# Performance work log

Hardware: AMD Instinct MI355X
Metric: run time of the kernel (lower is better)

Reference implementation:

```python
import jax, jax.numpy as jnp
import numpy as np

N_P, N_A, N_S, D = 50000, 25000, 1, 64
ALPHA = 0.2  # leaky_relu negative slope
E_P2P, E_P2A, E_A2P, E_A2A = 800000, 400000, 400000, 400000


def _gat(z_msg, wh_dst, aw, src, dst, n_dst):
    """Per-edge-type GAT: score = leaky_relu(attn_fc([z_src ; Wh_dst])),
    segment softmax over destination, weighted scatter-sum of z_src.
    Attention linear is split into src/dst halves and applied per-node (cheaper)."""
    d = z_msg.shape[1]
    e = (z_msg @ aw[:d])[src] + (wh_dst @ aw[d:])[dst]  # [E]
    e = jnp.where(e > 0, e, ALPHA * e)                   # leaky_relu
    m = jax.ops.segment_max(e, dst, num_segments=n_dst)
    ex = jnp.exp(e - m[dst])
    den = jax.ops.segment_sum(ex, dst, num_segments=n_dst)
    w = ex / den[dst]                                    # per-dst softmax (mailbox softmax)
    return jax.ops.segment_sum(w[:, None] * z_msg[src], dst, num_segments=n_dst)


def setup_inputs() -> dict:
    ks = jax.random.split(jax.random.key(0), 32)
    sc = 1.0 / np.sqrt(D)
    f32, i32 = jnp.float32, jnp.int32
    inp = {
        "feat_P": jax.random.normal(ks[0], (N_P, D), f32),
        "feat_A": jax.random.normal(ks[1], (N_A, D), f32),
        "feat_state": jax.random.normal(ks[2], (N_S, D), f32),
    }
    for i, n in enumerate(["P", "A", "p2p", "p2a", "a2p", "a2a", "p2s", "a2s", "in"]):
        inp["W_" + n] = jax.random.normal(ks[3 + i], (D, D), f32) * sc
        inp["b_" + n] = jnp.zeros((D,), f32)
    for i, n in enumerate(["p2p", "p2a", "a2p", "a2a", "p2s", "a2s"]):
        inp["a_" + n] = jax.random.normal(ks[12 + i], (2 * D,), f32) * sc
    inp["src_p2p"] = jax.random.randint(ks[18], (E_P2P,), 0, N_P, i32)
    inp["dst_p2p"] = jax.random.randint(ks[19], (E_P2P,), 0, N_P, i32)
    inp["src_p2a"] = jax.random.randint(ks[20], (E_P2A,), 0, N_P, i32)
    inp["dst_p2a"] = jax.random.randint(ks[21], (E_P2A,), 0, N_A, i32)
    inp["src_a2p"] = jax.random.randint(ks[22], (E_A2P,), 0, N_A, i32)
    inp["dst_a2p"] = jax.random.randint(ks[23], (E_A2P,), 0, N_P, i32)
    inp["src_a2a"] = jax.random.randint(ks[24], (E_A2A,), 0, N_A, i32)
    inp["dst_a2a"] = jax.random.randint(ks[25], (E_A2A,), 0, N_A, i32)
    inp["src_p2s"] = jnp.arange(N_P, dtype=i32)
    inp["dst_p2s"] = jnp.zeros((N_P,), i32)
    inp["src_a2s"] = jnp.arange(N_A, dtype=i32)
    inp["dst_a2s"] = jnp.zeros((N_A,), i32)
    return inp


def reference(feat_P, feat_A, feat_state,
              W_P, b_P, W_A, b_A, W_p2p, b_p2p, W_p2a, b_p2a, W_a2p, b_a2p,
              W_a2a, b_a2a, W_p2s, b_p2s, W_a2s, b_a2s, W_in, b_in,
              a_p2p, a_p2a, a_a2p, a_a2a, a_p2s, a_a2s,
              src_p2p, dst_p2p, src_p2a, dst_p2a, src_a2p, dst_a2p,
              src_a2a, dst_a2a, src_p2s, dst_p2s, src_a2s, dst_a2s):
    Wh_P = feat_P @ W_P + b_P          # self transform per node type
    Wh_A = feat_A @ W_A + b_A
    Wh_in = feat_state @ W_in + b_in   # 'in' self-loop message to state
    h_P = jax.nn.relu(
        Wh_P
        + _gat(feat_P @ W_p2p + b_p2p, Wh_P, a_p2p, src_p2p, dst_p2p, N_P)
        + _gat(feat_A @ W_a2p + b_a2p, Wh_P, a_a2p, src_a2p, dst_a2p, N_P))
    h_A = jax.nn.relu(
        Wh_A
        + _gat(feat_P @ W_p2a + b_p2a, Wh_A, a_p2a, src_p2a, dst_p2a, N_A)
        + _gat(feat_A @ W_a2a + b_a2a, Wh_A, a_a2a, src_a2a, dst_a2a, N_A))
    h_S = jax.nn.relu(
        Wh_in
        + _gat(feat_P @ W_p2s + b_p2s, Wh_in, a_p2s, src_p2s, dst_p2s, N_S)
        + _gat(feat_A @ W_a2s + b_a2s, Wh_in, a_a2s, src_a2s, dst_a2s, N_S))
    return (h_P, h_A, h_S)
```

## Files before the change

### kernel.cpp

```cpp
#include <hip/hip_runtime.h>
#include <math.h>

#define ALPHA 0.2f
#define NP 50000
#define NA 25000
#define NBINS 150000
#define ABASE 100000
#define NBUCK 586
#define CH 4096
#define CAP 8192
#define GP ((NP + 63) / 64)
#define GA ((NA + 63) / 64)
#define GATB ((NP + NA) / 4)
#define SNB_P 128
#define SNB_A 64
#define SNB (SNB_P + SNB_A)

typedef unsigned short u16;
typedef __attribute__((ext_vector_type(8))) short bf16x8;
typedef __attribute__((ext_vector_type(8))) unsigned short u16x8;
typedef __attribute__((ext_vector_type(4))) float f32x4;

__device__ __forceinline__ float bf2f(u16 u) { return __uint_as_float(((unsigned)u) << 16); }
__device__ __forceinline__ u16 f2bf(float f) {
    unsigned x = __float_as_uint(f);
    return (u16)((x + 0x7fffu + ((x >> 16) & 1u)) >> 16);
}

struct FrontArgs {
    const float *feat_P, *feat_A, *feat_S;
    const float *W_P, *b_P, *W_A, *b_A, *W_p2p, *b_p2p, *W_p2a, *b_p2a,
                *W_a2p, *b_a2p, *W_a2a, *b_a2a, *W_p2s, *b_p2s, *W_a2s, *b_a2s,
                *W_in, *b_in;
    const float *a_p2p, *a_p2a, *a_a2p, *a_a2a, *a_p2s, *a_a2s;
    float *WhP, *WhA;
    u16 *z_p2p, *z_p2a, *z_p2s, *z_a2p, *z_a2a, *z_a2s;
    float *ss_p2p, *sd_p2p, *ss_p2a, *sd_p2a, *ss_a2p, *sd_a2p, *ss_a2a, *sd_a2a,
          *ss_p2s, *ss_a2s;
    float *sdst2, *outS, *den2, *numP, *numA;
    int *done;
};

__device__ __forceinline__ void xform_body(int bid,
    const float* __restrict__ X, int N,
    const float* __restrict__ W0, const float* __restrict__ b0, float* __restrict__ Wh,
    const float* __restrict__ dA, float* __restrict__ sdA,
    const float* __restrict__ dB, float* __restrict__ sdB,
    const float* __restrict__ W1, const float* __restrict__ b1, u16* __restrict__ z1,
    const float* __restrict__ v1, float* __restrict__ s1,
    const float* __restrict__ W2, const float* __restrict__ b2, u16* __restrict__ z2,
    const float* __restrict__ v2, float* __restrict__ s2,
    const float* __restrict__ W3, const float* __restrict__ b3, u16* __restrict__ z3,
    const float* __restrict__ v3, float* __restrict__ s3)
{
    int tid = threadIdx.x, wv = tid >> 6, lane = tid & 63;
    int g = lane >> 4, li = lane & 15;
    const float* Wm = wv == 0 ? W0 : wv == 1 ? W1 : wv == 2 ? W2 : W3;
    const float* bm = wv == 0 ? b0 : wv == 1 ? b1 : wv == 2 ? b2 : b3;
    const float* dv = wv == 0 ? dA : wv == 1 ? v1 : wv == 2 ? v2 : v3;
    float* sm       = wv == 0 ? sdA : wv == 1 ? s1 : wv == 2 ? s2 : s3;
    u16* zm         = wv == 1 ? z1 : wv == 2 ? z2 : wv == 3 ? z3 : nullptr;

    bf16x8 Bf[4][2];
#pragma unroll
    for (int cb = 0; cb < 4; ++cb)
#pragma unroll
        for (int kc = 0; kc < 2; ++kc) {
            bf16x8 t;
#pragma unroll
            for (int j = 0; j < 8; ++j)
                t[j] = (short)f2bf(Wm[(kc * 32 + g * 8 + j) * 64 + cb * 16 + li]);
            Bf[cb][kc] = t;
        }
    float bl[4], dvl[4], dbl[4];
#pragma unroll
    for (int cb = 0; cb < 4; ++cb) {
        bl[cb]  = bm[cb * 16 + li];
        dvl[cb] = dv[cb * 16 + li];
        dbl[cb] = (wv == 0) ? dB[cb * 16 + li] : 0.f;
    }

    int base0 = bid * 64;
#pragma unroll
    for (int rt = 0; rt < 4; ++rt) {
        int rbase = base0 + rt * 16;
        if (rbase >= N) break;
        int rowC = min(rbase + li, N - 1);
        bf16x8 Af[2];
#pragma unroll
        for (int kc = 0; kc < 2; ++kc) {
            const float* xp = X + (long long)rowC * 64 + kc * 32 + g * 8;
            float4 x0 = *(const float4*)xp;
            float4 x1 = *(const float4*)(xp + 4);
            bf16x8 t;
            t[0] = (short)f2bf(x0.x); t[1] = (short)f2bf(x0.y);
            t[2] = (short)f2bf(x0.z); t[3] = (short)f2bf(x0.w);
            t[4] = (short)f2bf(x1.x); t[5] = (short)f2bf(x1.y);
            t[6] = (short)f2bf(x1.z); t[7] = (short)f2bf(x1.w);
            Af[kc] = t;
        }
        f32x4 acc[4] = {{0,0,0,0},{0,0,0,0},{0,0,0,0},{0,0,0,0}};
#pragma unroll
        for (int kc = 0; kc < 2; ++kc)
#pragma unroll
            for (int cb = 0; cb < 4; ++cb)
                acc[cb] = __builtin_amdgcn_mfma_f32_16x16x32_bf16(Af[kc], Bf[cb][kc], acc[cb], 0, 0, 0);
        float pd[4] = {0,0,0,0}, pb[4] = {0,0,0,0};
#pragma unroll
        for (int cb = 0; cb < 4; ++cb)
#pragma unroll
            for (int r = 0; r < 4; ++r) {
                float val = acc[cb][r] + bl[cb];
                acc[cb][r] = val;
                pd[r] = fmaf(val, dvl[cb], pd[r]);
                pb[r] = fmaf(val, dbl[cb], pb[r]);
            }
#pragma unroll
        for (int o = 1; o < 16; o <<= 1)
#pragma unroll
            for (int r = 0; r < 4; ++r) {
                pd[r] += __shfl_xor(pd[r], o, 64);
                pb[r] += __shfl_xor(pb[r], o, 64);
            }
        int rg = rbase + g * 4;
        if (li == 0) {
#pragma unroll
            for (int r = 0; r < 4; ++r) {
                int row = rg + r;
                if (row < N) {
                    sm[row] = pd[r];
                    if (wv == 0) sdB[row] = pb[r];
                }
            }
        }
        if (wv == 0) {
#pragma unroll
            for (int r = 0; r < 4; ++r) {
                int row = rg + r;
                if (row < N)
#pragma unroll
                    for (int cb = 0; cb < 4; ++cb)
                        Wh[(long long)row * 64 + cb * 16 + li] = acc[cb][r];
            }
        } else {
#pragma unroll
            for (int r = 0; r < 4; ++r) {
                int row = rg + r;
                if (row < N)
#pragma unroll
                    for (int cb = 0; cb < 4; ++cb)
                        zm[(long long)row * 64 + cb * 16 + li] = f2bf(acc[cb][r]);
            }
        }
    }
}

__device__ __forceinline__ void edge_decode(int k,
    const int* __restrict__ s0, const int* __restrict__ d0, int E0,
    const int* __restrict__ s1, const int* __restrict__ d1, int E1,
    const int* __restrict__ s2, const int* __restrict__ d2, int E2,
    const int* __restrict__ s3, const int* __restrict__ d3,
    int& src, int& bin) {
    if (k < E0) { src = s0[k]; bin = 2 * d0[k]; return; }
    k -= E0; if (k < E1) { src = s1[k]; bin = 2 * d1[k] + 1; return; }
    k -= E1; if (k < E2) { src = s2[k]; bin = ABASE + 2 * d2[k]; return; }
    k -= E2; src = s3[k]; bin = ABASE + 2 * d3[k] + 1;
}

__global__ __launch_bounds__(256) void fused_front(FrontArgs A) {
    int bid = blockIdx.x;
    int tid = threadIdx.x;
    if (bid < GP) {
        xform_body(bid, A.feat_P, NP,
                   A.W_P, A.b_P, A.WhP, A.a_p2p + 64, A.sd_p2p, A.a_a2p + 64, A.sd_a2p,
                   A.W_p2p, A.b_p2p, A.z_p2p, A.a_p2p, A.ss_p2p,
                   A.W_p2a, A.b_p2a, A.z_p2a, A.a_p2a, A.ss_p2a,
                   A.W_p2s, A.b_p2s, A.z_p2s, A.a_p2s, A.ss_p2s);
        return;
    }
    bid -= GP;
    if (bid < GA) {
        xform_body(bid, A.feat_A, NA,
                   A.W_A, A.b_A, A.WhA, A.a_p2a + 64, A.sd_p2a, A.a_a2a + 64, A.sd_a2a,
                   A.W_a2p, A.b_a2p, A.z_a2p, A.a_a2p, A.ss_a2p,
                   A.W_a2a, A.b_a2a, A.z_a2a, A.a_a2a, A.ss_a2a,
                   A.W_a2s, A.b_a2s, A.z_a2s, A.a_a2s, A.ss_a2s);
        return;
    }
    if (tid < 64) {
        int c = tid;
        float acc = A.b_in[c];
        for (int k = 0; k < 64; ++k) acc = fmaf(A.feat_S[k], A.W_in[k * 64 + c], acc);
        A.outS[c] = acc;
        float v0 = acc * A.a_p2s[64 + c];
        float v1 = acc * A.a_a2s[64 + c];
#pragma unroll
        for (int off = 32; off > 0; off >>= 1) {
            v0 += __shfl_down(v0, off, 64);
            v1 += __shfl_down(v1, off, 64);
        }
        if (c == 0) { A.sdst2[0] = v0; A.sdst2[1] = v1; }
    } else if (tid < 128) A.numP[tid - 64] = 0.f;
    else if (tid < 192)   A.numA[tid - 128] = 0.f;
    else if (tid == 192)  A.den2[0] = 0.f;
    else if (tid == 193)  A.den2[1] = 0.f;
    else if (tid == 194)  *A.done = 0;
}

__global__ __launch_bounds__(256) void passA_scatter(
    const int* __restrict__ s0, const int* __restrict__ d0, int E0,
    const int* __restrict__ s1, const int* __restrict__ d1, int E1,
    const int* __restrict__ s2, const int* __restrict__ d2, int E2,
    const int* __restrict__ s3, const int* __restrict__ d3, int E3,
    int* __restrict__ cursor0, int Etot, int* __restrict__ ebuf) {
    __shared__ int h[NBUCK];
    __shared__ int base[NBUCK];
    int tid = threadIdx.x;
    for (int i = tid; i < NBUCK; i += 256) h[i] = 0;
    __syncthreads();
    int b0 = blockIdx.x * CH;
    int b1 = min(b0 + CH, Etot);
    int cbin[16], csrc[16];
#pragma unroll
    for (int it = 0; it < 16; ++it) {
        int i = b0 + it * 256 + tid;
        int bin = -1, src = 0;
        if (i < b1)
            edge_decode(i, s0, d0, E0, s1, d1, E1, s2, d2, E2, s3, d3, src, bin);
        cbin[it] = bin; csrc[it] = src;
        if (bin >= 0) atomicAdd(&h[bin >> 8], 1);
    }
    __syncthreads();
    for (int i = tid; i < NBUCK; i += 256) {
        int c = h[i];
        base[i] = c ? (i * CAP + atomicAdd(&cursor0[i], c)) : 0;
        h[i] = 0;
    }
    __syncthreads();
#pragma unroll
    for (int it = 0; it < 16; ++it) {
        int bin = cbin[it];
        if (bin >= 0) {
            int bk = bin >> 8;
            int pos = base[bk] + atomicAdd(&h[bk], 1);
            if (pos < (bk + 1) * CAP)
                ebuf[pos] = csrc[it] | ((bin & 255) << 16);
        }
    }
}

__global__ __launch_bounds__(256) void fine_sort(
    const int* __restrict__ ebuf, const int* __restrict__ cursor0,
    int* __restrict__ ssrc, int* __restrict__ offs) {
    __shared__ int lsrc[CAP];
    __shared__ int lcnt[256];
    __shared__ int loff[256];
    __shared__ int lcur[256];
    __shared__ int wtot[4];
    int b = blockIdx.x;
    int tid = threadIdx.x, lane = tid & 63, wv = tid >> 6;
    int bstart = b * CAP;
    int cnt = min(cursor0[b], CAP);
    int bend = bstart + cnt;
    lcnt[tid] = 0;
    __syncthreads();
    for (int e = bstart + tid; e < bend; e += 256)
        atomicAdd(&lcnt[((unsigned)ebuf[e]) >> 16], 1);
    __syncthreads();
    int v = lcnt[tid];
    int x = v;
#pragma unroll
    for (int o = 1; o < 64; o <<= 1) {
        int y = __shfl_up(x, o, 64);
        if (lane >= o) x += y;
    }
    if (lane == 63) wtot[wv] = x;
    __syncthreads();
    int woff = 0;
    for (int j = 0; j < wv; ++j) woff += wtot[j];
    int excl = x + woff - v;
    loff[tid] = excl;
    lcur[tid] = excl;
    __syncthreads();
    for (int e = bstart + tid; e < bend; e += 256) {
        int val = ebuf[e];
        int pos = atomicAdd(&lcur[((unsigned)val) >> 16], 1);
        lsrc[pos] = val & 0xFFFF;
    }
    __syncthreads();
    for (int i = tid; i < cnt; i += 256) ssrc[bstart + i] = lsrc[i];
    offs[b * 257 + tid] = bstart + loff[tid];
    if (tid == 0) offs[b * 257 + 256] = bend;
}

__device__ __forceinline__ void seg_gat_g8(const int* __restrict__ ssrc, int s0, int s1,
                                           const float* __restrict__ ss, float sd,
                                           const u16* __restrict__ z, int lane,
                                           float* __restrict__ acc) {
    int cnt = s1 - s0;
    if (cnt <= 0) return;
    int egrp = lane >> 3, cg8 = (lane & 7) * 8;
    float den = 0.f;
    for (int i = s0 + lane; i < s1; i += 64) {
        float e = ss[ssrc[i]] + sd; e = e > 0.f ? e : ALPHA * e; den += __expf(e);
    }
#pragma unroll
    for (int o = 32; o > 0; o >>= 1) den += __shfl_xor(den, o, 64);
    float inv = 1.f / den;
    for (int c = s0; c < s1; c += 64) {
        int i = c + lane; int s = 0; float w = 0.f;
        if (i < s1) {
            s = ssrc[i];
            float e = ss[s] + sd; e = e > 0.f ? e : ALPHA * e;
            w = __expf(e) * inv;
        }
        int cc = min(64, s1 - c);
        int nit = (cc + 7) >> 3;
        for (int it = 0; it < nit; ++it) {
            int ei = it * 8 + egrp;
            float wt = __shfl(w, ei, 64);
            int   st = __shfl(s, ei, 64);
            u16x8 q = *(const u16x8*)(z + (long long)st * 64 + cg8);
#pragma unroll
            for (int j = 0; j < 8; ++j)
                acc[j] = fmaf(wt, bf2f(q[j]), acc[j]);
        }
    }
}

__global__ __launch_bounds__(256) void fused_back(
    const int* __restrict__ ssrc, const int* __restrict__ offs,
    const float* __restrict__ WhP, float* __restrict__ outP,
    const float* __restrict__ WhA, float* __restrict__ outA,
    const float* __restrict__ ss_p2p, const float* __restrict__ sd_p2p, const u16* __restrict__ z_p2p,
    const float* __restrict__ ss_a2p, const float* __restrict__ sd_a2p, const u16* __restrict__ z_a2p,
    const float* __restrict__ ss_p2a, const float* __restrict__ sd_p2a, const u16* __restrict__ z_p2a,
    const float* __restrict__ ss_a2a, const float* __restrict__ sd_a2a, const u16* __restrict__ z_a2a,
    const int* __restrict__ srcP, const float* __restrict__ ssP, const u16* __restrict__ zP, int EP,
    const int* __restrict__ srcA, const float* __restrict__ ssA, const u16* __restrict__ zA, int EA,
    const float* __restrict__ sdst2, float* __restrict__ numP, float* __restrict__ numA,
    float* __restrict__ den2, int* __restrict__ done, float* __restrict__ outS) {
    int tid = threadIdx.x, lane = tid & 63, wv = tid >> 6;
    if ((int)blockIdx.x >= SNB) {
        int g = ((int)blockIdx.x - SNB) * 4 + wv;
        bool isP = g < NP;
        int d = isP ? g : g - NP;
        int bin0 = isP ? 2 * d : ABASE + 2 * d;
        int obase = (bin0 >> 8) * 257 + (bin0 & 255);
        int e0 = offs[obase], e1 = offs[obase + 1], e2 = offs[obase + 2];
        int cnt = e2 - e0, c1 = e1 - e0;
        const float* ss0 = isP ? ss_p2p : ss_p2a;
        const float* ss1 = isP ? ss_a2p : ss_a2a;
        const u16* z0 = isP ? z_p2p : z_p2a;
        const u16* z1 = isP ? z_a2p : z_a2a;
        float sd0v = (isP ? sd_p2p : sd_p2a)[d];
        float sd1v = (isP ? sd_a2p : sd_a2a)[d];
        int egrp = lane >> 3, cg8 = (lane & 7) * 8;
        float acc[8] = {0.f, 0.f, 0.f, 0.f, 0.f, 0.f, 0.f, 0.f};
        if (cnt <= 64) {
            int s = 0; float w = 0.f;
            bool s1f = lane >= c1;
            if (lane < cnt) {
                s = ssrc[e0 + lane];
                float sc = (s1f ? ss1[s] : ss0[s]) + (s1f ? sd1v : sd0v);
                sc = sc > 0.f ? sc : ALPHA * sc;
                w = __expf(sc);
            }
            float d0 = s1f ? 0.f : w, d1 = s1f ? w : 0.f;
#pragma unroll
            for (int o = 32; o > 0; o >>= 1) {
                d0 += __shfl_xor(d0, o, 64);
                d1 += __shfl_xor(d1, o, 64);
            }
            float inv0 = 1.f / d0, inv1 = 1.f / d1;
            w = (lane < cnt) ? w * (s1f ? inv1 : inv0) : 0.f;
            int nit = (cnt + 7) >> 3;
            float wtv[8]; int stv[8]; u16x8 q[8];
#pragma unroll
            for (int it = 0; it < 8; ++it)
                if (it < nit) {
                    int ei = it * 8 + egrp;
                    wtv[it] = __shfl(w, ei, 64);
                    stv[it] = __shfl(s, ei, 64);
                }
#pragma unroll
            for (int it = 0; it < 8; ++it)
                if (it < nit) {
                    const u16* zp = (it * 8 + egrp >= c1) ? z1 : z0;
                    q[it] = *(const u16x8*)(zp + (long long)stv[it] * 64 + cg8);
                }
#pragma unroll
            for (int it = 0; it < 8; ++it)
                if (it < nit) {
#pragma unroll
                    for (int j = 0; j < 8; ++j)
                        acc[j] = fmaf(wtv[it], bf2f(q[it][j]), acc[j]);
                }
        } else {
            seg_gat_g8(ssrc, e0, e1, ss0, sd0v, z0, lane, acc);
            seg_gat_g8(ssrc, e1, e2, ss1, sd1v, z1, lane, acc);
        }
#pragma unroll
        for (int o = 8; o <= 32; o <<= 1)
#pragma unroll
            for (int j = 0; j < 8; ++j)
                acc[j] += __shfl_xor(acc[j], o, 64);
        if (lane < 8) {
            const float* Wh = isP ? WhP : WhA;
            float* outp = isP ? outP : outA;
            const float* sp = &Wh[(long long)d * 64 + lane * 8];
            float4 s0v = *(const float4*)sp;
            float4 s1v = *(const float4*)(sp + 4);
            float4 r0, r1;
            r0.x = fmaxf(s0v.x + acc[0], 0.f); r0.y = fmaxf(s0v.y + acc[1], 0.f);
            r0.z = fmaxf(s0v.z + acc[2], 0.f); r0.w = fmaxf(s0v.w + acc[3], 0.f);
            r1.x = fmaxf(s1v.x + acc[4], 0.f); r1.y = fmaxf(s1v.y + acc[5], 0.f);
            r1.z = fmaxf(s1v.z + acc[6], 0.f); r1.w = fmaxf(s1v.w + acc[7], 0.f);
            float* op = &outp[(long long)d * 64 + lane * 8];
            *(float4*)op = r0;
            *(float4*)(op + 4) = r1;
        }
        return;
    }
    __shared__ float red[4][64];
    __shared__ float dred[4];
    __shared__ int tick;
    int sb = blockIdx.x;
    bool isP = sb < SNB_P;
    const int* src = isP ? srcP : srcA;
    const float* ss = isP ? ssP : ssA;
    const u16* z = isP ? zP : zA;
    int E = isP ? EP : EA;
    float sdst = sdst2[isP ? 0 : 1];
    float* num = isP ? numP : numA;
    int bidl = isP ? sb : sb - SNB_P;
    int nb = isP ? SNB_P : SNB_A;
    int egrp = lane >> 3, cg8 = (lane & 7) * 8;
    int gw = bidl * 4 + wv;
    int waves = nb * 4;
    float acc[8] = {0,0,0,0,0,0,0,0};
    float dpart = 0.f;
    for (int base = gw * 8; base < E; base += waves * 8) {
        int i = base + egrp;
        float w = 0.f; int ri = 0;
        if (i < E) {
            ri = src[i];
            float e = ss[ri] + sdst;
            e = e > 0.f ? e : ALPHA * e;
            w = __expf(e);
        }
        dpart += w;
        u16x8 q = *(const u16x8*)(z + (long long)ri * 64 + cg8);
#pragma unroll
        for (int j = 0; j < 8; ++j)
            acc[j] = fmaf(w, bf2f(q[j]), acc[j]);
    }
#pragma unroll
    for (int o = 8; o <= 32; o <<= 1)
#pragma unroll
        for (int j = 0; j < 8; ++j)
            acc[j] += __shfl_xor(acc[j], o, 64);
#pragma unroll
    for (int o = 32; o > 0; o >>= 1) dpart += __shfl_xor(dpart, o, 64);
    if (lane < 8)
#pragma unroll
        for (int j = 0; j < 8; ++j) red[wv][lane * 8 + j] = acc[j];
    if (lane == 0) dred[wv] = dpart;
    __syncthreads();
    if (tid < 64) {
        float t = red[0][tid] + red[1][tid] + red[2][tid] + red[3][tid];
        atomicAdd(&num[tid], t);
    }
    if (tid == 64) {
        float dtot = (dred[0] + dred[1] + dred[2] + dred[3]) * 0.125f;
        atomicAdd(&den2[isP ? 0 : 1], dtot);
    }
    __threadfence();
    __syncthreads();
    if (tid == 0) tick = atomicAdd(done, 1);
    __syncthreads();
    if (tick == SNB - 1 && tid < 64) {
        float dP = __hip_atomic_load(&den2[0], __ATOMIC_ACQUIRE, __HIP_MEMORY_SCOPE_AGENT);
        float dA = __hip_atomic_load(&den2[1], __ATOMIC_ACQUIRE, __HIP_MEMORY_SCOPE_AGENT);
        float nP = __hip_atomic_load(&numP[tid], __ATOMIC_ACQUIRE, __HIP_MEMORY_SCOPE_AGENT);
        float nA = __hip_atomic_load(&numA[tid], __ATOMIC_ACQUIRE, __HIP_MEMORY_SCOPE_AGENT);
        float whin = outS[tid];
        outS[tid] = fmaxf(whin + nP / dP + nA / dA, 0.f);
    }
}

extern "C" void kernel_launch(void* const* d_in, const int* in_sizes, int n_in,
                              void* d_out, int out_size, void* d_ws, size_t ws_size,
                              hipStream_t stream) {
    const float* feat_P = (const float*)d_in[0];
    const float* feat_A = (const float*)d_in[1];
    const float* feat_S = (const float*)d_in[2];
    const float* W_P   = (const float*)d_in[3];  const float* b_P   = (const float*)d_in[4];
    const float* W_A   = (const float*)d_in[5];  const float* b_A   = (const float*)d_in[6];
    const float* W_p2p = (const float*)d_in[7];  const float* b_p2p = (const float*)d_in[8];
    const float* W_p2a = (const float*)d_in[9];  const float* b_p2a = (const float*)d_in[10];
    const float* W_a2p = (const float*)d_in[11]; const float* b_a2p = (const float*)d_in[12];
    const float* W_a2a = (const float*)d_in[13]; const float* b_a2a = (const float*)d_in[14];
    const float* W_p2s = (const float*)d_in[15]; const float* b_p2s = (const float*)d_in[16];
    const float* W_a2s = (const float*)d_in[17]; const float* b_a2s = (const float*)d_in[18];
    const float* W_in  = (const float*)d_in[19]; const float* b_in  = (const float*)d_in[20];
    const float* a_p2p = (const float*)d_in[21];
    const float* a_p2a = (const float*)d_in[22];
    const float* a_a2p = (const float*)d_in[23];
    const float* a_a2a = (const float*)d_in[24];
    const float* a_p2s = (const float*)d_in[25];
    const float* a_a2s = (const float*)d_in[26];
    const int* src_p2p = (const int*)d_in[27]; const int* dst_p2p = (const int*)d_in[28];
    const int* src_p2a = (const int*)d_in[29]; const int* dst_p2a = (const int*)d_in[30];
    const int* src_a2p = (const int*)d_in[31]; const int* dst_a2p = (const int*)d_in[32];
    const int* src_a2a = (const int*)d_in[33]; const int* dst_a2a = (const int*)d_in[34];
    const int* src_p2s = (const int*)d_in[35];
    const int* src_a2s = (const int*)d_in[37];
    int E_p2p = in_sizes[27], E_p2a = in_sizes[29], E_a2p = in_sizes[31], E_a2a = in_sizes[33];
    int E_p2s = in_sizes[35], E_a2s = in_sizes[37];
    int E_tot = E_p2p + E_a2p + E_p2a + E_a2a;

    float* out = (float*)d_out;
    float* outP = out;
    float* outA = out + (long long)NP * 64;
    float* outS = out + (long long)(NP + NA) * 64;

    float* ws = (float*)d_ws;
    float* WhP = ws; ws += (long long)NP * 64;
    float* WhA = ws; ws += (long long)NA * 64;
    u16* z_p2p = (u16*)ws; ws += (long long)NP * 32;
    u16* z_p2a = (u16*)ws; ws += (long long)NP * 32;
    u16* z_p2s = (u16*)ws; ws += (long long)NP * 32;
    u16* z_a2p = (u16*)ws; ws += (long long)NA * 32;
    u16* z_a2a = (u16*)ws; ws += (long long)NA * 32;
    u16* z_a2s = (u16*)ws; ws += (long long)NA * 32;
    float* ss_p2p = ws; ws += NP;  float* sd_p2p = ws; ws += NP;
    float* ss_p2a = ws; ws += NP;  float* sd_p2a = ws; ws += NA;
    float* ss_a2p = ws; ws += NA;  float* sd_a2p = ws; ws += NP;
    float* ss_a2a = ws; ws += NA;  float* sd_a2a = ws; ws += NA;
    float* ss_p2s = ws; ws += NP;
    float* ss_a2s = ws; ws += NA;
    float* sdst2  = ws; ws += 2;
    float* den2   = ws; ws += 2;
    float* numP   = ws; ws += 64;
    float* numA   = ws; ws += 64;
    int*   done   = (int*)ws; ws += 1;
    int* cursor0 = (int*)ws; ws += NBUCK;
    int* iw = (int*)ws;
    int* ebuf = iw; iw += NBUCK * CAP;
    int* ssrc = iw; iw += NBUCK * CAP;
    int* offs = iw; iw += NBUCK * 257 + 1;

    const int T = 256;
    int nblk = (E_tot + CH - 1) / CH;

    hipMemsetAsync(cursor0, 0, (size_t)NBUCK * 4, stream);

    FrontArgs FA;
    FA.feat_P = feat_P; FA.feat_A = feat_A; FA.feat_S = feat_S;
    FA.W_P = W_P; FA.b_P = b_P; FA.W_A = W_A; FA.b_A = b_A;
    FA.W_p2p = W_p2p; FA.b_p2p = b_p2p; FA.W_p2a = W_p2a; FA.b_p2a = b_p2a;
    FA.W_a2p = W_a2p; FA.b_a2p = b_a2p; FA.W_a2a = W_a2a; FA.b_a2a = b_a2a;
    FA.W_p2s = W_p2s; FA.b_p2s = b_p2s; FA.W_a2s = W_a2s; FA.b_a2s = b_a2s;
    FA.W_in = W_in; FA.b_in = b_in;
    FA.a_p2p = a_p2p; FA.a_p2a = a_p2a; FA.a_a2p = a_a2p; FA.a_a2a = a_a2a;
    FA.a_p2s = a_p2s; FA.a_a2s = a_a2s;
    FA.WhP = WhP; FA.WhA = WhA;
    FA.z_p2p = z_p2p; FA.z_p2a = z_p2a; FA.z_p2s = z_p2s;
    FA.z_a2p = z_a2p; FA.z_a2a = z_a2a; FA.z_a2s = z_a2s;
    FA.ss_p2p = ss_p2p; FA.sd_p2p = sd_p2p; FA.ss_p2a = ss_p2a; FA.sd_p2a = sd_p2a;
    FA.ss_a2p = ss_a2p; FA.sd_a2p = sd_a2p; FA.ss_a2a = ss_a2a; FA.sd_a2a = sd_a2a;
    FA.ss_p2s = ss_p2s; FA.ss_a2s = ss_a2s;
    FA.sdst2 = sdst2; FA.outS = outS; FA.den2 = den2; FA.numP = numP; FA.numA = numA;
    FA.done = done;
    fused_front<<<GP + GA + 1, T, 0, stream>>>(FA);

    passA_scatter<<<nblk, T, 0, stream>>>(src_p2p, dst_p2p, E_p2p,
                                          src_a2p, dst_a2p, E_a2p,
                                          src_p2a, dst_p2a, E_p2a,
                                          src_a2a, dst_a2a, E_a2a,
                                          cursor0, E_tot, ebuf);
    fine_sort<<<NBUCK, T, 0, stream>>>(ebuf, cursor0, ssrc, offs);

    fused_back<<<SNB + GATB, T, 0, stream>>>(ssrc, offs,
        WhP, outP, WhA, outA,
        ss_p2p, sd_p2p, z_p2p, ss_a2p, sd_a2p, z_a2p,
        ss_p2a, sd_p2a, z_p2a, ss_a2a, sd_a2a, z_a2a,
        src_p2s, ss_p2s, z_p2s, E_p2s,
        src_a2s, ss_a2s, z_a2s, E_a2s,
        sdst2, numP, numA, den2, done, outS);
}
```

Before: 144.6 us.

## Fuse edge bucket scatter into front transform kernel; simplify per-dst GAT path

```diff
diff --git a/kernel.cpp b/kernel.cpp
--- a/kernel.cpp
+++ b/kernel.cpp
@@ -39,6 +39,10 @@
           *ss_p2s, *ss_a2s;
     float *sdst2, *outS, *den2, *numP, *numA;
     int *done;
+    const int *src_p2p, *dst_p2p, *src_a2p, *dst_a2p,
+              *src_p2a, *dst_p2a, *src_a2a, *dst_a2a;
+    int E_p2p, E_a2p, E_p2a, E_a2a, E_tot, nblk;
+    int *cursor0, *ebuf;
 };
 
 __device__ __forceinline__ void xform_body(int bid,
@@ -168,8 +172,48 @@
 }
 
 __global__ __launch_bounds__(256) void fused_front(FrontArgs A) {
+    __shared__ int h[NBUCK];
+    __shared__ int base[NBUCK];
     int bid = blockIdx.x;
     int tid = threadIdx.x;
+    if (bid < A.nblk) {
+        for (int i = tid; i < NBUCK; i += 256) h[i] = 0;
+        __syncthreads();
+        int b0 = bid * CH;
+        int b1 = min(b0 + CH, A.E_tot);
+        int cbin[16], csrc[16];
+#pragma unroll
+        for (int it = 0; it < 16; ++it) {
+            int i = b0 + it * 256 + tid;
+            int bin = -1, src = 0;
+            if (i < b1)
+                edge_decode(i, A.src_p2p, A.dst_p2p, A.E_p2p,
+                            A.src_a2p, A.dst_a2p, A.E_a2p,
+                            A.src_p2a, A.dst_p2a, A.E_p2a,
+                            A.src_a2a, A.dst_a2a, src, bin);
+            cbin[it] = bin; csrc[it] = src;
+            if (bin >= 0) atomicAdd(&h[bin >> 8], 1);
+        }
+        __syncthreads();
+        for (int i = tid; i < NBUCK; i += 256) {
+            int c = h[i];
+            base[i] = c ? (i * CAP + atomicAdd(&A.cursor0[i], c)) : 0;
+            h[i] = 0;
+        }
+        __syncthreads();
+#pragma unroll
+        for (int it = 0; it < 16; ++it) {
+            int bin = cbin[it];
+            if (bin >= 0) {
+                int bk = bin >> 8;
+                int pos = base[bk] + atomicAdd(&h[bk], 1);
+                if (pos < (bk + 1) * CAP)
+                    A.ebuf[pos] = csrc[it] | ((bin & 255) << 16);
+            }
+        }
+        return;
+    }
+    bid -= A.nblk;
     if (bid < GP) {
         xform_body(bid, A.feat_P, NP,
                    A.W_P, A.b_P, A.WhP, A.a_p2p + 64, A.sd_p2p, A.a_a2p + 64, A.sd_a2p,
@@ -205,48 +249,6 @@
     else if (tid == 192)  A.den2[0] = 0.f;
     else if (tid == 193)  A.den2[1] = 0.f;
     else if (tid == 194)  *A.done = 0;
-}
-
-__global__ __launch_bounds__(256) void passA_scatter(
-    const int* __restrict__ s0, const int* __restrict__ d0, int E0,
-    const int* __restrict__ s1, const int* __restrict__ d1, int E1,
-    const int* __restrict__ s2, const int* __restrict__ d2, int E2,
-    const int* __restrict__ s3, const int* __restrict__ d3, int E3,
-    int* __restrict__ cursor0, int Etot, int* __restrict__ ebuf) {
-    __shared__ int h[NBUCK];
-    __shared__ int base[NBUCK];
-    int tid = threadIdx.x;
-    for (int i = tid; i < NBUCK; i += 256) h[i] = 0;
-    __syncthreads();
-    int b0 = blockIdx.x * CH;
-    int b1 = min(b0 + CH, Etot);
-    int cbin[16], csrc[16];
-#pragma unroll
-    for (int it = 0; it < 16; ++it) {
-        int i = b0 + it * 256 + tid;
-        int bin = -1, src = 0;
-        if (i < b1)
-            edge_decode(i, s0, d0, E0, s1, d1, E1, s2, d2, E2, s3, d3, src, bin);
-        cbin[it] = bin; csrc[it] = src;
-        if (bin >= 0) atomicAdd(&h[bin >> 8], 1);
-    }
-    __syncthreads();
-    for (int i = tid; i < NBUCK; i += 256) {
-        int c = h[i];
-        base[i] = c ? (i * CAP + atomicAdd(&cursor0[i], c)) : 0;
-        h[i] = 0;
-    }
-    __syncthreads();
-#pragma unroll
-    for (int it = 0; it < 16; ++it) {
-        int bin = cbin[it];
-        if (bin >= 0) {
-            int bk = bin >> 8;
-            int pos = base[bk] + atomicAdd(&h[bk], 1);
-            if (pos < (bk + 1) * CAP)
-                ebuf[pos] = csrc[it] | ((bin & 255) << 16);
-        }
-    }
 }
 
 __global__ __launch_bounds__(256) void fine_sort(
@@ -300,22 +302,19 @@
     int cnt = s1 - s0;
     if (cnt <= 0) return;
     int egrp = lane >> 3, cg8 = (lane & 7) * 8;
-    float den = 0.f;
-    for (int i = s0 + lane; i < s1; i += 64) {
-        float e = ss[ssrc[i]] + sd; e = e > 0.f ? e : ALPHA * e; den += __expf(e);
-    }
-#pragma unroll
-    for (int o = 32; o > 0; o >>= 1) den += __shfl_xor(den, o, 64);
-    float inv = 1.f / den;
-    for (int c = s0; c < s1; c += 64) {
-        int i = c + lane; int s = 0; float w = 0.f;
-        if (i < s1) {
-            s = ssrc[i];
-            float e = ss[s] + sd; e = e > 0.f ? e : ALPHA * e;
-            w = __expf(e) * inv;
-        }
-        int cc = min(64, s1 - c);
-        int nit = (cc + 7) >> 3;
+    if (cnt <= 64) {
+        int s = 0; float w = 0.f;
+        if (lane < cnt) {
+            s = ssrc[s0 + lane];
+            float e = ss[s] + sd;
+            e = e > 0.f ? e : ALPHA * e;
+            w = __expf(e);
+        }
+        float den = w;
+#pragma unroll
+        for (int o = 32; o > 0; o >>= 1) den += __shfl_xor(den, o, 64);
+        w *= 1.f / den;
+        int nit = (cnt + 7) >> 3;
         for (int it = 0; it < nit; ++it) {
             int ei = it * 8 + egrp;
             float wt = __shfl(w, ei, 64);
@@ -324,6 +323,33 @@
 #pragma unroll
             for (int j = 0; j < 8; ++j)
                 acc[j] = fmaf(wt, bf2f(q[j]), acc[j]);
+        }
+    } else {
+        float den = 0.f;
+        for (int i = s0 + lane; i < s1; i += 64) {
+            float e = ss[ssrc[i]] + sd; e = e > 0.f ? e : ALPHA * e; den += __expf(e);
+        }
+#pragma unroll
+        for (int o = 32; o > 0; o >>= 1) den += __shfl_xor(den, o, 64);
+        float inv = 1.f / den;
+        for (int c = s0; c < s1; c += 64) {
+            int i = c + lane; int s = 0; float w = 0.f;
+            if (i < s1) {
+                s = ssrc[i];
+                float e = ss[s] + sd; e = e > 0.f ? e : ALPHA * e;
+                w = __expf(e) * inv;
+            }
+            int cc = min(64, s1 - c);
+            int nit = (cc + 7) >> 3;
+            for (int it = 0; it < nit; ++it) {
+                int ei = it * 8 + egrp;
+                float wt = __shfl(w, ei, 64);
+                int   st = __shfl(s, ei, 64);
+                u16x8 q = *(const u16x8*)(z + (long long)st * 64 + cg8);
+#pragma unroll
+                for (int j = 0; j < 8; ++j)
+                    acc[j] = fmaf(wt, bf2f(q[j]), acc[j]);
+            }
         }
     }
 }
@@ -348,58 +374,15 @@
         int bin0 = isP ? 2 * d : ABASE + 2 * d;
         int obase = (bin0 >> 8) * 257 + (bin0 & 255);
         int e0 = offs[obase], e1 = offs[obase + 1], e2 = offs[obase + 2];
-        int cnt = e2 - e0, c1 = e1 - e0;
         const float* ss0 = isP ? ss_p2p : ss_p2a;
         const float* ss1 = isP ? ss_a2p : ss_a2a;
         const u16* z0 = isP ? z_p2p : z_p2a;
         const u16* z1 = isP ? z_a2p : z_a2a;
         float sd0v = (isP ? sd_p2p : sd_p2a)[d];
         float sd1v = (isP ? sd_a2p : sd_a2a)[d];
-        int egrp = lane >> 3, cg8 = (lane & 7) * 8;
         float acc[8] = {0.f, 0.f, 0.f, 0.f, 0.f, 0.f, 0.f, 0.f};
-        if (cnt <= 64) {
-            int s = 0; float w = 0.f;
-            bool s1f = lane >= c1;
-            if (lane < cnt) {
-                s = ssrc[e0 + lane];
-                float sc = (s1f ? ss1[s] : ss0[s]) + (s1f ? sd1v : sd0v);
-                sc = sc > 0.f ? sc : ALPHA * sc;
-                w = __expf(sc);
-            }
-            float d0 = s1f ? 0.f : w, d1 = s1f ? w : 0.f;
-#pragma unroll
-            for (int o = 32; o > 0; o >>= 1) {
-                d0 += __shfl_xor(d0, o, 64);
-                d1 += __shfl_xor(d1, o, 64);
-            }
-            float inv0 = 1.f / d0, inv1 = 1.f / d1;
-            w = (lane < cnt) ? w * (s1f ? inv1 : inv0) : 0.f;
-            int nit = (cnt + 7) >> 3;
-            float wtv[8]; int stv[8]; u16x8 q[8];
-#pragma unroll
-            for (int it = 0; it < 8; ++it)
-                if (it < nit) {
-                    int ei = it * 8 + egrp;
-                    wtv[it] = __shfl(w, ei, 64);
-                    stv[it] = __shfl(s, ei, 64);
-                }
-#pragma unroll
-            for (int it = 0; it < 8; ++it)
-                if (it < nit) {
-                    const u16* zp = (it * 8 + egrp >= c1) ? z1 : z0;
-                    q[it] = *(const u16x8*)(zp + (long long)stv[it] * 64 + cg8);
-                }
-#pragma unroll
-            for (int it = 0; it < 8; ++it)
-                if (it < nit) {
-#pragma unroll
-                    for (int j = 0; j < 8; ++j)
-                        acc[j] = fmaf(wtv[it], bf2f(q[it][j]), acc[j]);
-                }
-        } else {
-            seg_gat_g8(ssrc, e0, e1, ss0, sd0v, z0, lane, acc);
-            seg_gat_g8(ssrc, e1, e2, ss1, sd1v, z1, lane, acc);
-        }
+        seg_gat_g8(ssrc, e0, e1, ss0, sd0v, z0, lane, acc);
+        seg_gat_g8(ssrc, e1, e2, ss1, sd1v, z1, lane, acc);
 #pragma unroll
         for (int o = 8; o <= 32; o <<= 1)
 #pragma unroll
@@ -573,13 +556,13 @@
     FA.ss_p2s = ss_p2s; FA.ss_a2s = ss_a2s;
     FA.sdst2 = sdst2; FA.outS = outS; FA.den2 = den2; FA.numP = numP; FA.numA = numA;
     FA.done = done;
-    fused_front<<<GP + GA + 1, T, 0, stream>>>(FA);
-
-    passA_scatter<<<nblk, T, 0, stream>>>(src_p2p, dst_p2p, E_p2p,
-                                          src_a2p, dst_a2p, E_a2p,
-                                          src_p2a, dst_p2a, E_p2a,
-                                          src_a2a, dst_a2a, E_a2a,
-                                          cursor0, E_tot, ebuf);
+    FA.src_p2p = src_p2p; FA.dst_p2p = dst_p2p; FA.src_a2p = src_a2p; FA.dst_a2p = dst_a2p;
+    FA.src_p2a = src_p2a; FA.dst_p2a = dst_p2a; FA.src_a2a = src_a2a; FA.dst_a2a = dst_a2a;
+    FA.E_p2p = E_p2p; FA.E_a2p = E_a2p; FA.E_p2a = E_p2a; FA.E_a2a = E_a2a;
+    FA.E_tot = E_tot; FA.nblk = nblk;
+    FA.cursor0 = cursor0; FA.ebuf = ebuf;
+    fused_front<<<nblk + GP + GA + 1, T, 0, stream>>>(FA);
+
     fine_sort<<<NBUCK, T, 0, stream>>>(ebuf, cursor0, ssrc, offs);
 
     fused_back<<<SNB + GATB, T, 0, stream>>>(ssrc, offs,
```

Result: no change. 145.2 us (+0.4%).
